# Performance work log

Hardware: AMD Instinct MI355X
Metric: run time of the kernel (lower is better)

The kernel has to match this reference:

```python
import jax, jax.numpy as jnp
import numpy as np

UNITS = 512
GROUPS = 32
EPS = 1e-3  # keras GroupNormalization default epsilon


def group_norm(x, gamma, beta):
    # x: [B,H,W,C]; normalize over (H,W, channels-within-group)
    B, H, W, C = x.shape
    xg = x.reshape(B, H, W, GROUPS, C // GROUPS)
    mean = xg.mean(axis=(1, 2, 4), keepdims=True)
    var = xg.var(axis=(1, 2, 4), keepdims=True)
    xn = (xg - mean) * jax.lax.rsqrt(var + EPS)
    return xn.reshape(B, H, W, C) * gamma + beta


def setup_inputs() -> dict:
    key = jax.random.key(0)
    ks = jax.random.split(key, 6)
    B, H, W, C = 16, 32, 32, UNITS
    std = 0.02  # RandomNormal(stddev=0.02) kernel init
    return {
        "x": jax.random.normal(ks[0], (B, H, W, C), jnp.float32),
        "gamma": jnp.ones((C,), jnp.float32),
        "beta": jnp.zeros((C,), jnp.float32),
        "Wq": std * jax.random.normal(ks[1], (C, UNITS), jnp.float32),
        "bq": jnp.zeros((UNITS,), jnp.float32),
        "Wk": std * jax.random.normal(ks[2], (C, UNITS), jnp.float32),
        "bk": jnp.zeros((UNITS,), jnp.float32),
        "Wv": std * jax.random.normal(ks[3], (C, UNITS), jnp.float32),
        "bv": jnp.zeros((UNITS,), jnp.float32),
        "Wp": std * jax.random.normal(ks[4], (UNITS, UNITS), jnp.float32),
        "bp": jnp.zeros((UNITS,), jnp.float32),
    }


def reference(x, gamma, beta, Wq, bq, Wk, bk, Wv, bv, Wp, bp):
    B, H, W, C = x.shape
    scale = jnp.float32(UNITS) ** -0.5
    xn = group_norm(x, gamma, beta)  # note: original residual uses normalized input
    # flatten spatial dims to N = H*W tokens (same math as bhwc/bHWc einsums)
    xf = xn.reshape(B, H * W, C)
    q = xf @ Wq + bq
    k = xf @ Wk + bk
    v = xf @ Wv + bv
    scores = jnp.einsum('bnc,bmc->bnm', q, k) * scale  # [B, N, N]
    attn = jax.nn.softmax(scores, axis=-1)
    out = jnp.einsum('bnm,bmc->bnc', attn, v)
    proj = out @ Wp + bp
    return xn + proj.reshape(B, H, W, C)
```

## Files before the change

### kernel.cpp

```cpp
#include <hip/hip_runtime.h>
#include <math.h>

#define BATCH 16
#define NTOK  1024
#define CH    512
#define NGRP  32
#define GSZ   16
#define EPSV  1e-3f
#define MTOT  (BATCH*NTOK)
#define SCALE 0.04419417382415922f
#define SEXP  (SCALE*1.4426950408889634f)

typedef unsigned short u16;
typedef __attribute__((ext_vector_type(4))) float f32x4;
typedef __attribute__((ext_vector_type(8))) short s16x8;

__device__ __forceinline__ u16 f2bf(float f) {
    union { float f; unsigned u; } x{f};
    unsigned r = x.u + 0x7fff + ((x.u >> 16) & 1);
    return (u16)(r >> 16);
}

__device__ __forceinline__ void gld16(const u16* g, u16* l) {
    __builtin_amdgcn_global_load_lds(
        (const __attribute__((address_space(1))) void*)g,
        (__attribute__((address_space(3))) void*)l, 16, 0, 0);
}

#define MFMA16 __builtin_amdgcn_mfma_f32_16x16x32_bf16

__global__ __launch_bounds__(256) void gn_stats(const float* __restrict__ x,
                                                float2* __restrict__ stats) {
    int bg = blockIdx.x;
    int b = bg >> 5, g = bg & 31;
    const float* base = x + (size_t)b * NTOK * CH + g * GSZ;
    float s = 0.f, ss = 0.f;
    for (int i = threadIdx.x; i < 4096; i += 256) {
        int p = i >> 2, c4 = i & 3;
        float4 v = *(const float4*)(base + (size_t)p * CH + c4 * 4);
        s  += v.x + v.y + v.z + v.w;
        ss += v.x * v.x + v.y * v.y + v.z * v.z + v.w * v.w;
    }
    for (int off = 32; off; off >>= 1) {
        s  += __shfl_down(s, off);
        ss += __shfl_down(ss, off);
    }
    __shared__ float2 part[4];
    if ((threadIdx.x & 63) == 0) part[threadIdx.x >> 6] = make_float2(s, ss);
    __syncthreads();
    if (threadIdx.x == 0) {
        float S = 0.f, SS = 0.f;
        for (int i = 0; i < 4; i++) { S += part[i].x; SS += part[i].y; }
        float mean = S * (1.f / 16384.f);
        float var  = SS * (1.f / 16384.f) - mean * mean;
        stats[bg] = make_float2(mean, rsqrtf(var + EPSV));
    }
}

__global__ __launch_bounds__(256) void gn_apply(const float* __restrict__ x,
                                                const float2* __restrict__ stats,
                                                const float* __restrict__ gamma,
                                                const float* __restrict__ beta,
                                                float* __restrict__ xn,
                                                u16* __restrict__ xnb) {
    size_t total = (size_t)MTOT * CH / 4;
    for (size_t i4 = (size_t)blockIdx.x * 256 + threadIdx.x; i4 < total;
         i4 += (size_t)gridDim.x * 256) {
        size_t flat = i4 * 4;
        int c = (int)(flat & (CH - 1));
        int b = (int)(flat >> 19);
        int g = c >> 4;
        float2 st = stats[(b << 5) + g];
        float4 xv = *(const float4*)(x + flat);
        float4 gv = *(const float4*)(gamma + c);
        float4 bv = *(const float4*)(beta + c);
        float4 o;
        o.x = (xv.x - st.x) * st.y * gv.x + bv.x;
        o.y = (xv.y - st.x) * st.y * gv.y + bv.y;
        o.z = (xv.z - st.x) * st.y * gv.z + bv.z;
        o.w = (xv.w - st.x) * st.y * gv.w + bv.w;
        *(float4*)(xn + flat) = o;
        uint2 h;
        h.x = (unsigned)f2bf(o.x) | ((unsigned)f2bf(o.y) << 16);
        h.y = (unsigned)f2bf(o.z) | ((unsigned)f2bf(o.w) << 16);
        *(uint2*)(xnb + flat) = h;
    }
}

__global__ __launch_bounds__(256) void weights_prep(
    const float* __restrict__ Wq, const float* __restrict__ Wk,
    const float* __restrict__ Wv, const float* __restrict__ Wp,
    u16* __restrict__ WTqkv, u16* __restrict__ WTp) {
    int z = blockIdx.z;
    const float* src = z == 0 ? Wq : z == 1 ? Wk : z == 2 ? Wv : Wp;
    u16* dst = z < 3 ? WTqkv + (size_t)z * CH * CH : WTp;
    __shared__ u16 tile[64][66];
    int r0 = blockIdx.y * 64, c0 = blockIdx.x * 64;
    int t = threadIdx.x;
    for (int i = 0; i < 16; i++) {
        int idx = i * 256 + t;
        int r = idx >> 6, c = idx & 63;
        tile[r][c] = f2bf(src[(size_t)(r0 + r) * CH + c0 + c]);
    }
    __syncthreads();
    for (int i = 0; i < 16; i++) {
        int idx = i * 256 + t;
        int oc = idx >> 6, orr = idx & 63;
        dst[(size_t)(c0 + oc) * CH + r0 + orr] = tile[orr][oc];
    }
}

__global__ void prep_bias(const float* __restrict__ bq, const float* __restrict__ bk,
                          const float* __restrict__ bv, float* __restrict__ bqkv) {
    int t = blockIdx.x * 256 + threadIdx.x;
    bqkv[t] = t < 512 ? bq[t] : (t < 1024 ? bk[t - 512] : bv[t - 1024]);
}

__global__ __launch_bounds__(256) void vt_transpose(const u16* __restrict__ in,
                                                    u16* __restrict__ out,
                                                    int R, int C, int ldIn,
                                                    long sIn, long sOut) {
    __shared__ u16 tile[64][66];
    int z = blockIdx.z;
    in  += (size_t)z * sIn;
    out += (size_t)z * sOut;
    int r0 = blockIdx.y * 64, c0 = blockIdx.x * 64;
    int t = threadIdx.x;
    for (int i = 0; i < 16; i++) {
        int idx = i * 256 + t;
        int r = idx >> 6, c = idx & 63;
        tile[r][c] = in[(size_t)(r0 + r) * ldIn + c0 + c];
    }
    __syncthreads();
    for (int i = 0; i < 16; i++) {
        int idx = i * 256 + t;
        int oc = idx >> 6, orr = idx & 63;
        out[(size_t)(c0 + oc) * R + r0 + orr] = tile[orr][oc];
    }
}

template <bool BIAS, bool RES, bool OUTF32>
__global__ __launch_bounds__(256) void gemm_bt(
    const u16* __restrict__ A, const u16* __restrict__ B, void* __restrict__ Cout,
    const float* __restrict__ bias, const float* __restrict__ res,
    int K, int lda, int ldb, int ldc,
    long sA, long sB, long sC, float alpha) {
    __shared__ __align__(16) u16 Asm[8192];
    __shared__ __align__(16) u16 Bsm[8192];

    unsigned flat = blockIdx.x + gridDim.x * (blockIdx.y + gridDim.y * blockIdx.z);
    unsigned nb = gridDim.x * gridDim.y * gridDim.z;
    unsigned lf = (flat & 7) * (nb >> 3) + (flat >> 3);
    unsigned pb = gridDim.x * gridDim.y;
    unsigned bz = lf / pb, rem = lf - bz * pb;
    unsigned by = rem / gridDim.x, bx = rem - by * gridDim.x;

    A += (size_t)bz * sA;
    B += (size_t)bz * sB;
    size_t zc = (size_t)bz * sC;

    int t = threadIdx.x;
    int wave = t >> 6, lane = t & 63;
    int wm = wave >> 1, wn = wave & 1;
    int rowA0 = by * 128;
    int colB0 = bx * 128;

    int c16log = (lane & 3) ^ ((lane >> 3) & 3);
    const u16* aG[2]; const u16* bG[2]; u16* aL[2]; u16* bL[2];
#pragma unroll
    for (int j = 0; j < 2; j++) {
        int s = wave * 2 + j;
        int row = s * 16 + (lane >> 2);
        aL[j] = Asm + s * 512;
        bL[j] = Bsm + s * 512;
        aG[j] = A + (size_t)(rowA0 + row) * lda + c16log * 8;
        bG[j] = B + (size_t)(colB0 + row) * ldb + c16log * 8;
    }

    int kg = lane >> 4;
    int aoff[4], boff[4];
#pragma unroll
    for (int i = 0; i < 4; i++) {
        int ra = wm * 64 + i * 16 + (lane & 15);
        aoff[i] = ra * 32 + (kg ^ ((ra >> 1) & 3)) * 8;
        int rb = wn * 64 + i * 16 + (lane & 15);
        boff[i] = rb * 32 + (kg ^ ((rb >> 1) & 3)) * 8;
    }

#define STG_G(buf, ktE)                          \
    {                                            \
        gld16(aG[0] + (ktE), aL[0] + (buf) * 4096); \
        gld16(aG[1] + (ktE), aL[1] + (buf) * 4096); \
        gld16(bG[0] + (ktE), bL[0] + (buf) * 4096); \
        gld16(bG[1] + (ktE), bL[1] + (buf) * 4096); \
    }

    f32x4 acc[4][4] = {};
    int nk = K >> 5;
    STG_G(0, 0);
    __syncthreads();
    for (int kt = 0; kt < nk; kt++) {
        if (kt + 1 < nk) STG_G((kt + 1) & 1, (kt + 1) * 32);
        const u16* as = Asm + (kt & 1) * 4096;
        const u16* bs = Bsm + (kt & 1) * 4096;
        s16x8 af[4], bfr[4];
#pragma unroll
        for (int i = 0; i < 4; i++) {
            af[i]  = *(const s16x8*)(as + aoff[i]);
            bfr[i] = *(const s16x8*)(bs + boff[i]);
        }
#pragma unroll
        for (int mi = 0; mi < 4; mi++)
#pragma unroll
            for (int nj = 0; nj < 4; nj++)
                acc[mi][nj] = MFMA16(af[mi], bfr[nj], acc[mi][nj], 0, 0, 0);
        __syncthreads();
    }
#undef STG_G

    int r0 = rowA0 + wm * 64 + (lane >> 4) * 4;
    int c0c = colB0 + wn * 64 + (lane & 15);
#pragma unroll
    for (int mi = 0; mi < 4; mi++) {
#pragma unroll
        for (int nj = 0; nj < 4; nj++) {
            int c = c0c + nj * 16;
            float bv = BIAS ? bias[c] : 0.f;
            f32x4 v = acc[mi][nj];
#pragma unroll
            for (int j = 0; j < 4; j++) {
                int rr = r0 + mi * 16 + j;
                float val = v[j] * alpha + bv;
                if (RES) val += res[(size_t)rr * ldc + c];
                if (OUTF32) ((float*)Cout)[zc + (size_t)rr * ldc + c] = val;
                else        ((u16*)Cout)[zc + (size_t)rr * ldc + c] = f2bf(val);
            }
        }
    }
}

__global__ __launch_bounds__(512, 2) void attn_fused(const u16* __restrict__ qkv,
                                                     const u16* __restrict__ vtg,
                                                     u16* __restrict__ ao) {
    __shared__ __align__(16) u16 S[65536];

    unsigned flat = blockIdx.x;
    unsigned lf = (flat & 7) * 32 + (flat >> 3);
    int b = lf >> 4, mt = lf & 15;

    int t = threadIdx.x, w = t >> 6, lane = t & 63;
    int rt = w >> 2, ct = w & 3;
    int l15 = lane & 15, kg = lane >> 4;

    const u16* kbase = qkv + (size_t)b * NTOK * 1536 + CH;
    int c16log = (lane & 3) ^ ((lane >> 3) & 3);

    const u16* bG[8];
#pragma unroll
    for (int j = 0; j < 8; j++) {
        int row = (w * 8 + j) * 16 + (lane >> 2);
        bG[j] = kbase + (size_t)row * 1536 + c16log * 8;
    }
    const u16* qp[2];
#pragma unroll
    for (int rg = 0; rg < 2; rg++)
        qp[rg] = qkv + (size_t)(b * NTOK + mt * 64 + rt * 32 + rg * 16 + l15) * 1536 + kg * 8;

    int rbb = ct * 256 + l15;
    int boffb = rbb * 32 + ((kg ^ ((rbb >> 1) & 3)) << 3);

    f32x4 acc1[2][16];
#pragma unroll
    for (int rg = 0; rg < 2; rg++)
#pragma unroll
        for (int nj = 0; nj < 16; nj++) acc1[rg][nj] = f32x4{0.f, 0.f, 0.f, 0.f};

#define KSTG(buf, kt)                                                        \
    { _Pragma("unroll")                                                      \
      for (int j = 0; j < 8; j++)                                            \
          gld16(bG[j] + (kt) * 32, S + (buf) * 32768 + (w * 8 + j) * 512); }

    KSTG(0, 0);
    s16x8 aqc[2], aqn[2];
    aqc[0] = *(const s16x8*)(qp[0]);
    aqc[1] = *(const s16x8*)(qp[1]);
    __syncthreads();
#pragma unroll
    for (int kt = 0; kt < 16; kt++) {
        if (kt < 15) {
            KSTG((kt + 1) & 1, kt + 1);
            aqn[0] = *(const s16x8*)(qp[0] + (kt + 1) * 32);
            aqn[1] = *(const s16x8*)(qp[1] + (kt + 1) * 32);
        }
        const u16* bb = S + (kt & 1) * 32768;
#pragma unroll
        for (int nj = 0; nj < 16; nj++) {
            s16x8 bf = *(const s16x8*)(bb + boffb + nj * 512);
            acc1[0][nj] = MFMA16(aqc[0], bf, acc1[0][nj], 0, 0, 0);
            acc1[1][nj] = MFMA16(aqc[1], bf, acc1[1][nj], 0, 0, 0);
        }
        if (kt < 15) { aqc[0] = aqn[0]; aqc[1] = aqn[1]; }
        __syncthreads();
    }
#undef KSTG

    float* redm = (float*)S;
    float* reds = redm + 256;
    float mr[2][4], iv[2][4];
#pragma unroll
    for (int rg = 0; rg < 2; rg++)
#pragma unroll
        for (int j = 0; j < 4; j++) {
            float m = acc1[rg][0][j];
#pragma unroll
            for (int nj = 1; nj < 16; nj++) m = fmaxf(m, acc1[rg][nj][j]);
            for (int off = 1; off < 16; off <<= 1) m = fmaxf(m, __shfl_xor(m, off));
            mr[rg][j] = m;
        }
    if (l15 == 0) {
#pragma unroll
        for (int rg = 0; rg < 2; rg++)
#pragma unroll
            for (int j = 0; j < 4; j++)
                redm[(rt * 32 + rg * 16 + kg * 4 + j) * 4 + ct] = mr[rg][j];
    }
    __syncthreads();
#pragma unroll
    for (int rg = 0; rg < 2; rg++)
#pragma unroll
        for (int j = 0; j < 4; j++) {
            int row = rt * 32 + rg * 16 + kg * 4 + j;
            mr[rg][j] = fmaxf(fmaxf(redm[row * 4], redm[row * 4 + 1]),
                              fmaxf(redm[row * 4 + 2], redm[row * 4 + 3]));
        }
#pragma unroll
    for (int rg = 0; rg < 2; rg++)
#pragma unroll
        for (int j = 0; j < 4; j++) {
            float s = 0.f;
#pragma unroll
            for (int nj = 0; nj < 16; nj++) {
                float e = exp2f((acc1[rg][nj][j] - mr[rg][j]) * SEXP);
                acc1[rg][nj][j] = e;
                s += e;
            }
            for (int off = 1; off < 16; off <<= 1) s += __shfl_xor(s, off);
            if (l15 == 0) reds[(rt * 32 + rg * 16 + kg * 4 + j) * 4 + ct] = s;
        }
    __syncthreads();
#pragma unroll
    for (int rg = 0; rg < 2; rg++)
#pragma unroll
        for (int j = 0; j < 4; j++) {
            int row = rt * 32 + rg * 16 + kg * 4 + j;
            iv[rg][j] = 1.f / (reds[row * 4] + reds[row * 4 + 1] +
                               reds[row * 4 + 2] + reds[row * 4 + 3]);
        }
    __syncthreads();

#pragma unroll
    for (int rg = 0; rg < 2; rg++)
#pragma unroll
        for (int nj = 0; nj < 16; nj++) {
            int k = ct * 256 + nj * 16 + l15;
            int g = k >> 3, ko = k & 7;
#pragma unroll
            for (int j = 0; j < 4; j++) {
                int row = rt * 32 + rg * 16 + kg * 4 + j;
                S[row * 1024 + ((g ^ (row & 7)) << 3) + ko] =
                    f2bf(acc1[rg][nj][j] * iv[rg][j]);
            }
        }
    __syncthreads();

    f32x4 acc2[2][8];
#pragma unroll
    for (int rg = 0; rg < 2; rg++)
#pragma unroll
        for (int cj = 0; cj < 8; cj++) acc2[rg][cj] = f32x4{0.f, 0.f, 0.f, 0.f};

    const u16* vrow[8];
#pragma unroll
    for (int cj = 0; cj < 8; cj++)
        vrow[cj] = vtg + ((size_t)b * 512 + ct * 128 + cj * 16 + l15) * 1024 + kg * 8;

    int prowA[2] = {rt * 32 + l15, rt * 32 + 16 + l15};
    for (int c = 0; c < 32; c++) {
        s16x8 pa[2];
#pragma unroll
        for (int rg = 0; rg < 2; rg++) {
            int row = prowA[rg];
            pa[rg] = *(const s16x8*)(S + row * 1024 + (((c * 4 + kg) ^ (row & 7)) << 3));
        }
#pragma unroll
        for (int cj = 0; cj < 8; cj++) {
            s16x8 vf = *(const s16x8*)(vrow[cj] + c * 32);
            acc2[0][cj] = MFMA16(pa[0], vf, acc2[0][cj], 0, 0, 0);
            acc2[1][cj] = MFMA16(pa[1], vf, acc2[1][cj], 0, 0, 0);
        }
    }

    __syncthreads();
#pragma unroll
    for (int rg = 0; rg < 2; rg++)
#pragma unroll
        for (int cj = 0; cj < 8; cj++)
#pragma unroll
            for (int j = 0; j < 4; j++) {
                int row = rt * 32 + rg * 16 + kg * 4 + j;
                int ch = ct * 128 + cj * 16 + l15;
                S[row * 512 + ((((ch >> 3) ^ (row & 7))) << 3) + (ch & 7)] =
                    f2bf(acc2[rg][cj][j]);
            }
    __syncthreads();
    u16* aop = ao + (size_t)(b * NTOK + mt * 64) * 512;
#pragma unroll
    for (int i = 0; i < 8; i++) {
        int f = i * 512 + t;
        int row = f >> 6, g = f & 63;
        uint4 v = *(const uint4*)(S + row * 512 + g * 8);
        *(uint4*)(aop + (size_t)row * 512 + ((g ^ (row & 7)) << 3)) = v;
    }
}

extern "C" void kernel_launch(void* const* d_in, const int* in_sizes, int n_in,
                              void* d_out, int out_size, void* d_ws, size_t ws_size,
                              hipStream_t stream) {
    const float* x     = (const float*)d_in[0];
    const float* gamma = (const float*)d_in[1];
    const float* beta  = (const float*)d_in[2];
    const float* Wq    = (const float*)d_in[3];
    const float* bq    = (const float*)d_in[4];
    const float* Wk    = (const float*)d_in[5];
    const float* bk    = (const float*)d_in[6];
    const float* Wv    = (const float*)d_in[7];
    const float* bv    = (const float*)d_in[8];
    const float* Wp    = (const float*)d_in[9];
    const float* bp    = (const float*)d_in[10];
    float* out = (float*)d_out;

    const size_t SZ  = (size_t)MTOT * CH;
    const size_t NSZ = (size_t)NTOK * CH;

    char* p = (char*)d_ws;
    float*  xn    = (float*)p;   p += SZ * 4;
    u16*    xnb   = (u16*)p;     p += SZ * 2;
    u16*    qkvb  = (u16*)p;     p += (size_t)MTOT * 3 * CH * 2;
    u16*    vt    = (u16*)p;     p += SZ * 2;
    u16*    ao    = (u16*)p;     p += SZ * 2;
    u16*    WTqkv = (u16*)p;     p += (size_t)3 * CH * CH * 2;
    u16*    WTp   = (u16*)p;     p += (size_t)CH * CH * 2;
    float*  bqkv  = (float*)p;   p += 3 * CH * 4;
    float2* stats = (float2*)p;

    dim3 blk(256);

    gn_stats<<<BATCH * NGRP, blk, 0, stream>>>(x, stats);
    gn_apply<<<2048, blk, 0, stream>>>(x, stats, gamma, beta, xn, xnb);
    weights_prep<<<dim3(8, 8, 4), blk, 0, stream>>>(Wq, Wk, Wv, Wp, WTqkv, WTp);
    prep_bias<<<6, blk, 0, stream>>>(bq, bk, bv, bqkv);

    gemm_bt<true, false, false><<<dim3(12, 128, 1), blk, 0, stream>>>(
        xnb, WTqkv, qkvb, bqkv, nullptr, CH, CH, CH, 3 * CH, 0, 0, 0, 1.f);

    vt_transpose<<<dim3(8, 16, BATCH), blk, 0, stream>>>(
        qkvb + 2 * CH, vt, NTOK, CH, 3 * CH, (long)NTOK * 3 * CH, (long)NSZ);

    attn_fused<<<256, 512, 0, stream>>>(qkvb, vt, ao);

    gemm_bt<true, true, true><<<dim3(4, 128, 1), blk, 0, stream>>>(
        ao, WTp, out, bp, xn, CH, CH, CH, CH, 0, 0, 0, 1.f);
}
```

Measured before the change: 283.2 us.

## Halve attention query tile, drop LDS K staging, raise occupancy

The fused attention kernel now handles 32 query rows per block instead of 64, with all 8 waves splitting the key/channel dimension. Doubling the block count halves shared memory use and per-thread accumulators, which raises the occupancy bound to 4 blocks per CU. K fragments are loaded straight from global memory, replacing the double-buffered LDS staging and its per-step barriers, and s_setprio brackets the MFMA loops. The cost is that K and V are re-read twice as often across blocks, and direct global loads lose the explicit LDS prefetch overlap.

```diff
diff --git a/kernel.cpp b/kernel.cpp
--- a/kernel.cpp
+++ b/kernel.cpp
@@ -239,70 +239,47 @@
     }
 }
 
-__global__ __launch_bounds__(512, 2) void attn_fused(const u16* __restrict__ qkv,
+__global__ __launch_bounds__(512, 4) void attn_fused(const u16* __restrict__ qkv,
                                                      const u16* __restrict__ vtg,
                                                      u16* __restrict__ ao) {
-    __shared__ __align__(16) u16 S[65536];
+    __shared__ __align__(16) u16 S[32768];
 
     unsigned flat = blockIdx.x;
-    unsigned lf = (flat & 7) * 32 + (flat >> 3);
-    int b = lf >> 4, mt = lf & 15;
+    unsigned lf = (flat & 7) * 64 + (flat >> 3);
+    int b = lf >> 5, mt = lf & 31;
 
     int t = threadIdx.x, w = t >> 6, lane = t & 63;
-    int rt = w >> 2, ct = w & 3;
+    int ct = w;
     int l15 = lane & 15, kg = lane >> 4;
 
-    const u16* kbase = qkv + (size_t)b * NTOK * 1536 + CH;
-    int c16log = (lane & 3) ^ ((lane >> 3) & 3);
-
-    const u16* bG[8];
-#pragma unroll
-    for (int j = 0; j < 8; j++) {
-        int row = (w * 8 + j) * 16 + (lane >> 2);
-        bG[j] = kbase + (size_t)row * 1536 + c16log * 8;
-    }
     const u16* qp[2];
 #pragma unroll
     for (int rg = 0; rg < 2; rg++)
-        qp[rg] = qkv + (size_t)(b * NTOK + mt * 64 + rt * 32 + rg * 16 + l15) * 1536 + kg * 8;
-
-    int rbb = ct * 256 + l15;
-    int boffb = rbb * 32 + ((kg ^ ((rbb >> 1) & 3)) << 3);
-
-    f32x4 acc1[2][16];
-#pragma unroll
-    for (int rg = 0; rg < 2; rg++)
-#pragma unroll
-        for (int nj = 0; nj < 16; nj++) acc1[rg][nj] = f32x4{0.f, 0.f, 0.f, 0.f};
-
-#define KSTG(buf, kt)                                                        \
-    { _Pragma("unroll")                                                      \
-      for (int j = 0; j < 8; j++)                                            \
-          gld16(bG[j] + (kt) * 32, S + (buf) * 32768 + (w * 8 + j) * 512); }
-
-    KSTG(0, 0);
-    s16x8 aqc[2], aqn[2];
-    aqc[0] = *(const s16x8*)(qp[0]);
-    aqc[1] = *(const s16x8*)(qp[1]);
-    __syncthreads();
+        qp[rg] = qkv + (size_t)(b * NTOK + mt * 32 + rg * 16 + l15) * 1536 + kg * 8;
+    const u16* kp[8];
+#pragma unroll
+    for (int nj = 0; nj < 8; nj++)
+        kp[nj] = qkv + (size_t)(b * NTOK + ct * 128 + nj * 16 + l15) * 1536 + CH + kg * 8;
+
+    f32x4 acc1[2][8];
+#pragma unroll
+    for (int rg = 0; rg < 2; rg++)
+#pragma unroll
+        for (int nj = 0; nj < 8; nj++) acc1[rg][nj] = f32x4{0.f, 0.f, 0.f, 0.f};
+
 #pragma unroll
     for (int kt = 0; kt < 16; kt++) {
-        if (kt < 15) {
-            KSTG((kt + 1) & 1, kt + 1);
-            aqn[0] = *(const s16x8*)(qp[0] + (kt + 1) * 32);
-            aqn[1] = *(const s16x8*)(qp[1] + (kt + 1) * 32);
-        }
-        const u16* bb = S + (kt & 1) * 32768;
-#pragma unroll
-        for (int nj = 0; nj < 16; nj++) {
-            s16x8 bf = *(const s16x8*)(bb + boffb + nj * 512);
-            acc1[0][nj] = MFMA16(aqc[0], bf, acc1[0][nj], 0, 0, 0);
-            acc1[1][nj] = MFMA16(aqc[1], bf, acc1[1][nj], 0, 0, 0);
-        }
-        if (kt < 15) { aqc[0] = aqn[0]; aqc[1] = aqn[1]; }
-        __syncthreads();
-    }
-#undef KSTG
+        s16x8 a0 = *(const s16x8*)(qp[0] + kt * 32);
+        s16x8 a1 = *(const s16x8*)(qp[1] + kt * 32);
+        __builtin_amdgcn_s_setprio(1);
+#pragma unroll
+        for (int nj = 0; nj < 8; nj++) {
+            s16x8 bf = *(const s16x8*)(kp[nj] + kt * 32);
+            acc1[0][nj] = MFMA16(a0, bf, acc1[0][nj], 0, 0, 0);
+            acc1[1][nj] = MFMA16(a1, bf, acc1[1][nj], 0, 0, 0);
+        }
+        __builtin_amdgcn_s_setprio(0);
+    }
 
     float* redm = (float*)S;
     float* reds = redm + 256;
@@ -313,7 +290,7 @@
         for (int j = 0; j < 4; j++) {
             float m = acc1[rg][0][j];
 #pragma unroll
-            for (int nj = 1; nj < 16; nj++) m = fmaxf(m, acc1[rg][nj][j]);
+            for (int nj = 1; nj < 8; nj++) m = fmaxf(m, acc1[rg][nj][j]);
             for (int off = 1; off < 16; off <<= 1) m = fmaxf(m, __shfl_xor(m, off));
             mr[rg][j] = m;
         }
@@ -322,16 +299,18 @@
         for (int rg = 0; rg < 2; rg++)
 #pragma unroll
             for (int j = 0; j < 4; j++)
-                redm[(rt * 32 + rg * 16 + kg * 4 + j) * 4 + ct] = mr[rg][j];
+                redm[(rg * 16 + kg * 4 + j) * 8 + ct] = mr[rg][j];
     }
     __syncthreads();
 #pragma unroll
     for (int rg = 0; rg < 2; rg++)
 #pragma unroll
         for (int j = 0; j < 4; j++) {
-            int row = rt * 32 + rg * 16 + kg * 4 + j;
-            mr[rg][j] = fmaxf(fmaxf(redm[row * 4], redm[row * 4 + 1]),
-                              fmaxf(redm[row * 4 + 2], redm[row * 4 + 3]));
+            int row = rg * 16 + kg * 4 + j;
+            float m = redm[row * 8];
+#pragma unroll
+            for (int q = 1; q < 8; q++) m = fmaxf(m, redm[row * 8 + q]);
+            mr[rg][j] = m;
         }
 #pragma unroll
     for (int rg = 0; rg < 2; rg++)
@@ -339,83 +318,85 @@
         for (int j = 0; j < 4; j++) {
             float s = 0.f;
 #pragma unroll
-            for (int nj = 0; nj < 16; nj++) {
+            for (int nj = 0; nj < 8; nj++) {
                 float e = exp2f((acc1[rg][nj][j] - mr[rg][j]) * SEXP);
                 acc1[rg][nj][j] = e;
                 s += e;
             }
             for (int off = 1; off < 16; off <<= 1) s += __shfl_xor(s, off);
-            if (l15 == 0) reds[(rt * 32 + rg * 16 + kg * 4 + j) * 4 + ct] = s;
+            if (l15 == 0) reds[(rg * 16 + kg * 4 + j) * 8 + ct] = s;
         }
     __syncthreads();
 #pragma unroll
     for (int rg = 0; rg < 2; rg++)
 #pragma unroll
         for (int j = 0; j < 4; j++) {
-            int row = rt * 32 + rg * 16 + kg * 4 + j;
-            iv[rg][j] = 1.f / (reds[row * 4] + reds[row * 4 + 1] +
-                               reds[row * 4 + 2] + reds[row * 4 + 3]);
-        }
-    __syncthreads();
-
-#pragma unroll
-    for (int rg = 0; rg < 2; rg++)
-#pragma unroll
-        for (int nj = 0; nj < 16; nj++) {
-            int k = ct * 256 + nj * 16 + l15;
+            int row = rg * 16 + kg * 4 + j;
+            float s = reds[row * 8];
+#pragma unroll
+            for (int q = 1; q < 8; q++) s += reds[row * 8 + q];
+            iv[rg][j] = 1.f / s;
+        }
+    __syncthreads();
+
+#pragma unroll
+    for (int rg = 0; rg < 2; rg++)
+#pragma unroll
+        for (int nj = 0; nj < 8; nj++) {
+            int k = ct * 128 + nj * 16 + l15;
             int g = k >> 3, ko = k & 7;
 #pragma unroll
             for (int j = 0; j < 4; j++) {
-                int row = rt * 32 + rg * 16 + kg * 4 + j;
+                int row = rg * 16 + kg * 4 + j;
                 S[row * 1024 + ((g ^ (row & 7)) << 3) + ko] =
                     f2bf(acc1[rg][nj][j] * iv[rg][j]);
             }
         }
     __syncthreads();
 
-    f32x4 acc2[2][8];
-#pragma unroll
-    for (int rg = 0; rg < 2; rg++)
-#pragma unroll
-        for (int cj = 0; cj < 8; cj++) acc2[rg][cj] = f32x4{0.f, 0.f, 0.f, 0.f};
-
-    const u16* vrow[8];
-#pragma unroll
-    for (int cj = 0; cj < 8; cj++)
-        vrow[cj] = vtg + ((size_t)b * 512 + ct * 128 + cj * 16 + l15) * 1024 + kg * 8;
-
-    int prowA[2] = {rt * 32 + l15, rt * 32 + 16 + l15};
+    f32x4 acc2[2][4];
+#pragma unroll
+    for (int rg = 0; rg < 2; rg++)
+#pragma unroll
+        for (int cj = 0; cj < 4; cj++) acc2[rg][cj] = f32x4{0.f, 0.f, 0.f, 0.f};
+
+    const u16* vp[4];
+#pragma unroll
+    for (int cj = 0; cj < 4; cj++)
+        vp[cj] = vtg + (size_t)(b * 512 + ct * 64 + cj * 16 + l15) * 1024 + kg * 8;
+
+#pragma unroll 4
     for (int c = 0; c < 32; c++) {
-        s16x8 pa[2];
-#pragma unroll
-        for (int rg = 0; rg < 2; rg++) {
-            int row = prowA[rg];
-            pa[rg] = *(const s16x8*)(S + row * 1024 + (((c * 4 + kg) ^ (row & 7)) << 3));
-        }
-#pragma unroll
-        for (int cj = 0; cj < 8; cj++) {
-            s16x8 vf = *(const s16x8*)(vrow[cj] + c * 32);
-            acc2[0][cj] = MFMA16(pa[0], vf, acc2[0][cj], 0, 0, 0);
-            acc2[1][cj] = MFMA16(pa[1], vf, acc2[1][cj], 0, 0, 0);
-        }
-    }
-
-    __syncthreads();
-#pragma unroll
-    for (int rg = 0; rg < 2; rg++)
-#pragma unroll
-        for (int cj = 0; cj < 8; cj++)
+        s16x8 pa0 = *(const s16x8*)(S + (size_t)l15 * 1024 +
+                                    (((c * 4 + kg) ^ (l15 & 7)) << 3));
+        s16x8 pa1 = *(const s16x8*)(S + (size_t)(16 + l15) * 1024 +
+                                    (((c * 4 + kg) ^ (l15 & 7)) << 3));
+        __builtin_amdgcn_s_setprio(1);
+#pragma unroll
+        for (int cj = 0; cj < 4; cj++) {
+            s16x8 vf = *(const s16x8*)(vp[cj] + c * 32);
+            acc2[0][cj] = MFMA16(pa0, vf, acc2[0][cj], 0, 0, 0);
+            acc2[1][cj] = MFMA16(pa1, vf, acc2[1][cj], 0, 0, 0);
+        }
+        __builtin_amdgcn_s_setprio(0);
+    }
+
+    __syncthreads();
+#pragma unroll
+    for (int rg = 0; rg < 2; rg++)
+#pragma unroll
+        for (int cj = 0; cj < 4; cj++)
 #pragma unroll
             for (int j = 0; j < 4; j++) {
-                int row = rt * 32 + rg * 16 + kg * 4 + j;
-                int ch = ct * 128 + cj * 16 + l15;
+                int row = rg * 16 + kg * 4 + j;
+                int ch = ct * 64 + cj * 16 + l15;
                 S[row * 512 + ((((ch >> 3) ^ (row & 7))) << 3) + (ch & 7)] =
                     f2bf(acc2[rg][cj][j]);
             }
     __syncthreads();
-    u16* aop = ao + (size_t)(b * NTOK + mt * 64) * 512;
-#pragma unroll
-    for (int i = 0; i < 8; i++) {
+    u16* aop = ao + (size_t)(b * NTOK + mt * 32) * 512;
+#pragma unroll
+    for (int i = 0; i < 4; i++) {
         int f = i * 512 + t;
         int row = f >> 6, g = f & 63;
         uint4 v = *(const uint4*)(S + row * 512 + g * 8);
@@ -466,7 +447,7 @@
     vt_transpose<<<dim3(8, 16, BATCH), blk, 0, stream>>>(
         qkvb + 2 * CH, vt, NTOK, CH, 3 * CH, (long)NTOK * 3 * CH, (long)NSZ);
 
-    attn_fused<<<256, 512, 0, stream>>>(qkvb, vt, ao);
+    attn_fused<<<512, 512, 0, stream>>>(qkvb, vt, ao);
 
     gemm_bt<true, true, true><<<dim3(4, 128, 1), blk, 0, stream>>>(
         ao, WTp, out, bp, xn, CH, CH, CH, CH, 0, 0, 0, 1.f);
```

Result: slower. 336.3 us (+18.8%).

## Split attention PV into separate batched GEMM and fuse V transpose into QKV epilogue

Applied to the files above, without the earlier changes.

The QKV GEMM epilogue now writes V directly in transposed layout, which removes the standalone transpose kernel. The attention kernel now stops after softmax and writes the normalized probability matrix P (bf16, B×N×N) to global memory. A batched generic GEMM then computes P·V. This trades the in-kernel PV stage, which read V fragments straight from global memory, for a tiled GEMM, at the cost of writing and re-reading a 32 MB P buffer. It also raises wave priority around the QK MFMA loop.

```diff
diff --git a/kernel.cpp b/kernel.cpp
--- a/kernel.cpp
+++ b/kernel.cpp
@@ -116,33 +116,11 @@
     bqkv[t] = t < 512 ? bq[t] : (t < 1024 ? bk[t - 512] : bv[t - 1024]);
 }
 
-__global__ __launch_bounds__(256) void vt_transpose(const u16* __restrict__ in,
-                                                    u16* __restrict__ out,
-                                                    int R, int C, int ldIn,
-                                                    long sIn, long sOut) {
-    __shared__ u16 tile[64][66];
-    int z = blockIdx.z;
-    in  += (size_t)z * sIn;
-    out += (size_t)z * sOut;
-    int r0 = blockIdx.y * 64, c0 = blockIdx.x * 64;
-    int t = threadIdx.x;
-    for (int i = 0; i < 16; i++) {
-        int idx = i * 256 + t;
-        int r = idx >> 6, c = idx & 63;
-        tile[r][c] = in[(size_t)(r0 + r) * ldIn + c0 + c];
-    }
-    __syncthreads();
-    for (int i = 0; i < 16; i++) {
-        int idx = i * 256 + t;
-        int oc = idx >> 6, orr = idx & 63;
-        out[(size_t)(c0 + oc) * R + r0 + orr] = tile[orr][oc];
-    }
-}
-
-template <bool BIAS, bool RES, bool OUTF32>
+template <bool BIAS, bool RES, bool OUTF32, bool VTOUT>
 __global__ __launch_bounds__(256) void gemm_bt(
     const u16* __restrict__ A, const u16* __restrict__ B, void* __restrict__ Cout,
     const float* __restrict__ bias, const float* __restrict__ res,
+    u16* __restrict__ vtout,
     int K, int lda, int ldb, int ldc,
     long sA, long sB, long sC, float alpha) {
     __shared__ __align__(16) u16 Asm[8192];
@@ -227,21 +205,31 @@
             int c = c0c + nj * 16;
             float bv = BIAS ? bias[c] : 0.f;
             f32x4 v = acc[mi][nj];
-#pragma unroll
-            for (int j = 0; j < 4; j++) {
-                int rr = r0 + mi * 16 + j;
-                float val = v[j] * alpha + bv;
-                if (RES) val += res[(size_t)rr * ldc + c];
-                if (OUTF32) ((float*)Cout)[zc + (size_t)rr * ldc + c] = val;
-                else        ((u16*)Cout)[zc + (size_t)rr * ldc + c] = f2bf(val);
+            if (VTOUT && c >= 1024) {
+                int rr0 = r0 + mi * 16;
+                int ch = c - 1024, bb = rr0 >> 10, tok = rr0 & 1023;
+                ushort4 pk;
+                pk.x = f2bf(v[0] * alpha + bv);
+                pk.y = f2bf(v[1] * alpha + bv);
+                pk.z = f2bf(v[2] * alpha + bv);
+                pk.w = f2bf(v[3] * alpha + bv);
+                *(ushort4*)(vtout + ((size_t)(bb * 512 + ch)) * 1024 + tok) = pk;
+            } else {
+#pragma unroll
+                for (int j = 0; j < 4; j++) {
+                    int rr = r0 + mi * 16 + j;
+                    float val = v[j] * alpha + bv;
+                    if (RES) val += res[(size_t)rr * ldc + c];
+                    if (OUTF32) ((float*)Cout)[zc + (size_t)rr * ldc + c] = val;
+                    else        ((u16*)Cout)[zc + (size_t)rr * ldc + c] = f2bf(val);
+                }
             }
         }
     }
 }
 
 __global__ __launch_bounds__(512, 2) void attn_fused(const u16* __restrict__ qkv,
-                                                     const u16* __restrict__ vtg,
-                                                     u16* __restrict__ ao) {
+                                                     u16* __restrict__ P) {
     __shared__ __align__(16) u16 S[65536];
 
     unsigned flat = blockIdx.x;
@@ -293,12 +281,14 @@
             aqn[1] = *(const s16x8*)(qp[1] + (kt + 1) * 32);
         }
         const u16* bb = S + (kt & 1) * 32768;
+        __builtin_amdgcn_s_setprio(1);
 #pragma unroll
         for (int nj = 0; nj < 16; nj++) {
             s16x8 bf = *(const s16x8*)(bb + boffb + nj * 512);
             acc1[0][nj] = MFMA16(aqc[0], bf, acc1[0][nj], 0, 0, 0);
             acc1[1][nj] = MFMA16(aqc[1], bf, acc1[1][nj], 0, 0, 0);
         }
+        __builtin_amdgcn_s_setprio(0);
         if (kt < 15) { aqc[0] = aqn[0]; aqc[1] = aqn[1]; }
         __syncthreads();
     }
@@ -358,68 +348,34 @@
         }
     __syncthreads();
 
-#pragma unroll
-    for (int rg = 0; rg < 2; rg++)
-#pragma unroll
-        for (int nj = 0; nj < 16; nj++) {
-            int k = ct * 256 + nj * 16 + l15;
-            int g = k >> 3, ko = k & 7;
-#pragma unroll
-            for (int j = 0; j < 4; j++) {
-                int row = rt * 32 + rg * 16 + kg * 4 + j;
-                S[row * 1024 + ((g ^ (row & 7)) << 3) + ko] =
-                    f2bf(acc1[rg][nj][j] * iv[rg][j]);
-            }
-        }
-    __syncthreads();
-
-    f32x4 acc2[2][8];
-#pragma unroll
-    for (int rg = 0; rg < 2; rg++)
-#pragma unroll
-        for (int cj = 0; cj < 8; cj++) acc2[rg][cj] = f32x4{0.f, 0.f, 0.f, 0.f};
-
-    const u16* vrow[8];
-#pragma unroll
-    for (int cj = 0; cj < 8; cj++)
-        vrow[cj] = vtg + ((size_t)b * 512 + ct * 128 + cj * 16 + l15) * 1024 + kg * 8;
-
-    int prowA[2] = {rt * 32 + l15, rt * 32 + 16 + l15};
-    for (int c = 0; c < 32; c++) {
-        s16x8 pa[2];
-#pragma unroll
-        for (int rg = 0; rg < 2; rg++) {
-            int row = prowA[rg];
-            pa[rg] = *(const s16x8*)(S + row * 1024 + (((c * 4 + kg) ^ (row & 7)) << 3));
-        }
-#pragma unroll
-        for (int cj = 0; cj < 8; cj++) {
-            s16x8 vf = *(const s16x8*)(vrow[cj] + c * 32);
-            acc2[0][cj] = MFMA16(pa[0], vf, acc2[0][cj], 0, 0, 0);
-            acc2[1][cj] = MFMA16(pa[1], vf, acc2[1][cj], 0, 0, 0);
-        }
-    }
-
-    __syncthreads();
-#pragma unroll
-    for (int rg = 0; rg < 2; rg++)
-#pragma unroll
-        for (int cj = 0; cj < 8; cj++)
-#pragma unroll
-            for (int j = 0; j < 4; j++) {
-                int row = rt * 32 + rg * 16 + kg * 4 + j;
-                int ch = ct * 128 + cj * 16 + l15;
-                S[row * 512 + ((((ch >> 3) ^ (row & 7))) << 3) + (ch & 7)] =
-                    f2bf(acc2[rg][cj][j]);
-            }
-    __syncthreads();
-    u16* aop = ao + (size_t)(b * NTOK + mt * 64) * 512;
-#pragma unroll
-    for (int i = 0; i < 8; i++) {
-        int f = i * 512 + t;
-        int row = f >> 6, g = f & 63;
-        uint4 v = *(const uint4*)(S + row * 512 + g * 8);
-        *(uint4*)(aop + (size_t)row * 512 + ((g ^ (row & 7)) << 3)) = v;
+    size_t pbase = (size_t)b * NTOK * NTOK + (size_t)mt * 64 * NTOK;
+#pragma unroll
+    for (int h = 0; h < 2; h++) {
+        __syncthreads();
+        if ((ct >> 1) == h) {
+#pragma unroll
+            for (int rg = 0; rg < 2; rg++)
+#pragma unroll
+                for (int nj = 0; nj < 16; nj++) {
+                    int c = (ct & 1) * 256 + nj * 16 + l15;
+                    int c16 = c >> 3, cw = c & 7;
+#pragma unroll
+                    for (int j = 0; j < 4; j++) {
+                        int row = rt * 32 + rg * 16 + kg * 4 + j;
+                        int pc16 = c16 ^ ((row >> 2) & 7);
+                        S[row * 512 + pc16 * 8 + cw] = f2bf(acc1[rg][nj][j] * iv[rg][j]);
+                    }
+                }
+        }
+        __syncthreads();
+#pragma unroll
+        for (int i = 0; i < 8; i++) {
+            int flat16 = (i * 512 + t) * 8;
+            int row = flat16 >> 9, c = flat16 & 511;
+            int pc16 = (c >> 3) ^ ((row >> 2) & 7);
+            uint4 vv = *(const uint4*)(S + row * 512 + pc16 * 8);
+            *(uint4*)(P + pbase + (size_t)row * NTOK + h * 512 + c) = vv;
+        }
     }
 }
 
@@ -441,6 +397,7 @@
 
     const size_t SZ  = (size_t)MTOT * CH;
     const size_t NSZ = (size_t)NTOK * CH;
+    const size_t SCB = (size_t)NTOK * NTOK;
 
     char* p = (char*)d_ws;
     float*  xn    = (float*)p;   p += SZ * 4;
@@ -448,6 +405,7 @@
     u16*    qkvb  = (u16*)p;     p += (size_t)MTOT * 3 * CH * 2;
     u16*    vt    = (u16*)p;     p += SZ * 2;
     u16*    ao    = (u16*)p;     p += SZ * 2;
+    u16*    P     = (u16*)p;     p += (size_t)BATCH * SCB * 2;
     u16*    WTqkv = (u16*)p;     p += (size_t)3 * CH * CH * 2;
     u16*    WTp   = (u16*)p;     p += (size_t)CH * CH * 2;
     float*  bqkv  = (float*)p;   p += 3 * CH * 4;
@@ -460,14 +418,15 @@
     weights_prep<<<dim3(8, 8, 4), blk, 0, stream>>>(Wq, Wk, Wv, Wp, WTqkv, WTp);
     prep_bias<<<6, blk, 0, stream>>>(bq, bk, bv, bqkv);
 
-    gemm_bt<true, false, false><<<dim3(12, 128, 1), blk, 0, stream>>>(
-        xnb, WTqkv, qkvb, bqkv, nullptr, CH, CH, CH, 3 * CH, 0, 0, 0, 1.f);
-
-    vt_transpose<<<dim3(8, 16, BATCH), blk, 0, stream>>>(
-        qkvb + 2 * CH, vt, NTOK, CH, 3 * CH, (long)NTOK * 3 * CH, (long)NSZ);
-
-    attn_fused<<<256, 512, 0, stream>>>(qkvb, vt, ao);
-
-    gemm_bt<true, true, true><<<dim3(4, 128, 1), blk, 0, stream>>>(
-        ao, WTp, out, bp, xn, CH, CH, CH, CH, 0, 0, 0, 1.f);
-}
+    gemm_bt<true, false, false, true><<<dim3(12, 128, 1), blk, 0, stream>>>(
+        xnb, WTqkv, qkvb, bqkv, nullptr, vt, CH, CH, CH, 3 * CH, 0, 0, 0, 1.f);
+
+    attn_fused<<<256, 512, 0, stream>>>(qkvb, P);
+
+    gemm_bt<false, false, false, false><<<dim3(4, 8, BATCH), blk, 0, stream>>>(
+        P, vt, ao, nullptr, nullptr, nullptr, NTOK, NTOK, NTOK, CH,
+        (long)SCB, (long)NSZ, (long)NSZ, 1.f);
+
+    gemm_bt<true, true, true, false><<<dim3(4, 128, 1), blk, 0, stream>>>(
+        ao, WTp, out, bp, xn, nullptr, CH, CH, CH, CH, 0, 0, 0, 1.f);
+}
```

New measurement: 260.1 us. -8.2%, faster.
